# Optimization experiments

Hardware: AMD Instinct MI355X
Metric: run time of the kernel (lower is better)

Reference implementation:

```python
import jax, jax.numpy as jnp
import numpy as np
from jax import lax


def _lstm_layer(x_tmajor, Wi, Wh, b, c0, h0):
    """Run one LSTM layer over time-major input [T, B, F_in].

    Flax OptimizedLSTMCell math, gate order (i, f, g, o):
      gates = x @ Wi + h @ Wh + b
      c' = sigmoid(f) * c + sigmoid(i) * tanh(g)
      h' = sigmoid(o) * tanh(c')
    """
    F = Wh.shape[0]

    def step(carry, xt):
        c, h = carry
        gates = xt @ Wi + h @ Wh + b  # [B, 4F]
        i, f, g, o = jnp.split(gates, 4, axis=-1)
        c_new = jax.nn.sigmoid(f) * c + jax.nn.sigmoid(i) * jnp.tanh(g)
        h_new = jax.nn.sigmoid(o) * jnp.tanh(c_new)
        return (c_new, h_new), h_new

    (c_fin, h_fin), ys = lax.scan(step, (c0, h0), x_tmajor)
    return ys, c_fin, h_fin


def setup_inputs() -> dict:
    key = jax.random.key(0)
    kx, kwi, kwh = jax.random.split(key, 3)
    B, T, F, L = 16, 512, 1024, 2
    scale = 1.0 / np.sqrt(F)
    x = jax.random.normal(kx, (B, T, F), dtype=jnp.float32)
    Wi = jax.random.normal(kwi, (L, F, 4 * F), dtype=jnp.float32) * scale
    Wh = jax.random.normal(kwh, (L, F, 4 * F), dtype=jnp.float32) * scale
    b = jnp.zeros((L, 4 * F), dtype=jnp.float32)
    c0 = jnp.zeros((L, B, F), dtype=jnp.float32)
    h0 = jnp.zeros((L, B, F), dtype=jnp.float32)
    return {"x": x, "Wi": Wi, "Wh": Wh, "b": b, "c0": c0, "h0": h0}


def reference(x, Wi, Wh, b, c0, h0):
    # x: [B, T, F] -> time-major [T, B, F] for scan
    L = Wi.shape[0]
    h_seq = jnp.transpose(x, (1, 0, 2))
    c_finals, h_finals = [], []
    for l in range(L):  # small fixed layer count
        h_seq, c_f, h_f = _lstm_layer(h_seq, Wi[l], Wh[l], b[l], c0[l], h0[l])
        c_finals.append(c_f)
        h_finals.append(h_f)
    out = jnp.transpose(h_seq, (1, 0, 2))  # [B, T, F]
    return out, jnp.stack(c_finals), jnp.stack(h_finals)
```

## Files before the change

kernel.cpp:

```cpp
#include <hip/hip_runtime.h>

#define F1 1024
#define F4 4096
#define NB 16
#define NT 512
#define NWG 256

typedef float f32x4 __attribute__((ext_vector_type(4)));
typedef unsigned u32x4 __attribute__((ext_vector_type(4)));

__global__ __launch_bounds__(256) void gemm_xi(
    const float* __restrict__ A, const float* __restrict__ Wi,
    const float* __restrict__ bias, float* __restrict__ Xi, int a_batch_major)
{
    __shared__ __align__(16) float As[16][68];
    __shared__ __align__(16) float Bs[16][68];
    const int tid = threadIdx.x;
    const int n0 = blockIdx.x * 64;
    const int m0 = blockIdx.y * 64;

    const int lrow = tid >> 2, lkq = tid & 3;
    const int bkr = tid >> 4, bnq = tid & 15;
    const int tm = tid & 15, tn = tid >> 4;

    const int m_l = m0 + lrow;
    const float* arow;
    if (a_batch_major) {
        int t = m_l >> 4, b = m_l & 15;
        arow = A + (size_t)(b * NT + t) * F1;
    } else {
        arow = A + (size_t)m_l * F1;
    }

    float acc[4][4];
#pragma unroll
    for (int i = 0; i < 4; i++)
#pragma unroll
        for (int j = 0; j < 4; j++) acc[i][j] = 0.f;

    for (int kc = 0; kc < F1; kc += 16) {
        float4 a4 = *(const float4*)(arow + kc + lkq * 4);
        float4 b4 = *(const float4*)(Wi + (size_t)(kc + bkr) * F4 + n0 + bnq * 4);
        __syncthreads();
        As[lkq * 4 + 0][lrow] = a4.x;
        As[lkq * 4 + 1][lrow] = a4.y;
        As[lkq * 4 + 2][lrow] = a4.z;
        As[lkq * 4 + 3][lrow] = a4.w;
        *(float4*)&Bs[bkr][bnq * 4] = b4;
        __syncthreads();
#pragma unroll
        for (int k = 0; k < 16; k++) {
            const float4 av = *(const float4*)&As[k][tm * 4];
            const float4 bv = *(const float4*)&Bs[k][tn * 4];
            float a_[4] = {av.x, av.y, av.z, av.w};
            float b_[4] = {bv.x, bv.y, bv.z, bv.w};
#pragma unroll
            for (int i = 0; i < 4; i++)
#pragma unroll
                for (int j = 0; j < 4; j++)
                    acc[i][j] = fmaf(a_[i], b_[j], acc[i][j]);
        }
    }

    const int n = n0 + tn * 4;
    const int g = n >> 10;
    const int wgi = (n & 1023) >> 2;
    const int np = wgi * 16 + g * 4;
    const float4 bi = *(const float4*)(bias + n);
#pragma unroll
    for (int i = 0; i < 4; i++) {
        int m = m0 + tm * 4 + i;
        float4 o;
        o.x = acc[i][0] + bi.x;
        o.y = acc[i][1] + bi.y;
        o.z = acc[i][2] + bi.z;
        o.w = acc[i][3] + bi.w;
        *(float4*)(Xi + (size_t)m * F4 + np) = o;
    }
}

__global__ __launch_bounds__(512, 1) void lstm_recur(
    const float* __restrict__ Wh,
    const float* __restrict__ Xi,
    const float* __restrict__ c0,
    const float* __restrict__ h0,
    float* __restrict__ Hb,
    unsigned* __restrict__ flags,
    unsigned tbase,
    float* __restrict__ hseq,
    long long st_t, long long st_b,
    float* __restrict__ cfin, float* __restrict__ hfin)
{
    const int tid = threadIdx.x;
    const int wg = blockIdx.x;

    const int ks = tid >> 4;
    const int rb = (tid >> 2) & 3;
    const int g = tid & 3;

    __shared__ __align__(16) f32x4 hbuf4[16 * 257];
    __shared__ __align__(16) f32x4 red4[32 * 65];
    __shared__ float gbuf[16 * 20];

    float wh[32][4];
    {
        const float* wp = Wh + (size_t)(ks * 32) * F4 + g * F1 + wg * 4;
#pragma unroll
        for (int kk = 0; kk < 32; kk++) {
            float4 w4 = *(const float4*)(wp + (size_t)kk * F4);
            wh[kk][0] = w4.x; wh[kk][1] = w4.y; wh[kk][2] = w4.z; wh[kk][3] = w4.w;
        }
    }

    const int ab = tid >> 2, aj = tid & 3;
    float creg = 0.f;
    if (tid < 64) creg = c0[ab * F1 + wg * 4 + aj];

    for (int t = 0; t < NT; ++t) {
        f32x4 vv[8];
        if (t == 0) {
#pragma unroll
            for (int c = 0; c < 8; ++c) {
                int f4 = c * 512 + tid;
                vv[c] = *((const f32x4*)h0 + f4);
            }
        } else {
            const f32x4* hsrc = (const f32x4*)(Hb + (size_t)(t & 1) * (NB * F1));
#pragma unroll
            for (int c = 0; c < 8; ++c) {
                int f4 = c * 512 + tid;
                asm volatile("global_load_dwordx4 %0, %1, off sc1"
                             : "=v"(vv[c]) : "v"(hsrc + f4));
            }
            asm volatile("s_waitcnt vmcnt(0)" ::: "memory");
        }
#pragma unroll
        for (int c = 0; c < 8; ++c) {
            int f4 = c * 512 + tid;
            int r = f4 >> 8, k4 = f4 & 255;
            hbuf4[r * 257 + (k4 ^ ((k4 >> 3) & 7))] = vv[c];
        }
        float xiv = 0.f;
        if (tid < 256) {
            int r = tid >> 4, c = tid & 15;
            xiv = Xi[(size_t)(t * NB + r) * F4 + wg * 16 + c];
        }
        __syncthreads();

        float acc[4][4];
#pragma unroll
        for (int i = 0; i < 4; i++) {
            acc[i][0] = 0.f; acc[i][1] = 0.f; acc[i][2] = 0.f; acc[i][3] = 0.f;
        }
#pragma unroll
        for (int s = 0; s < 8; ++s) {
            const int k4 = (ks << 3) + s;
            const int slot = k4 ^ ((k4 >> 3) & 7);
            f32x4 hv[4];
#pragma unroll
            for (int i = 0; i < 4; i++) hv[i] = hbuf4[(rb * 4 + i) * 257 + slot];
#pragma unroll
            for (int i = 0; i < 4; i++) {
#pragma unroll
                for (int j = 0; j < 4; j++) {
                    acc[i][j] = fmaf(hv[i].x, wh[s * 4 + 0][j], acc[i][j]);
                    acc[i][j] = fmaf(hv[i].y, wh[s * 4 + 1][j], acc[i][j]);
                    acc[i][j] = fmaf(hv[i].z, wh[s * 4 + 2][j], acc[i][j]);
                    acc[i][j] = fmaf(hv[i].w, wh[s * 4 + 3][j], acc[i][j]);
                }
            }
        }
#pragma unroll
        for (int i = 0; i < 4; i++)
            red4[ks * 65 + (rb * 4 + i) * 4 + g] =
                (f32x4){acc[i][0], acc[i][1], acc[i][2], acc[i][3]};
        __syncthreads();

        if (tid < 256) {
            const float* rf = (const float*)red4;
            float s = xiv;
#pragma unroll
            for (int kss = 0; kss < 32; ++kss) s += rf[kss * 260 + tid];
            int r = tid >> 4, c = tid & 15;
            gbuf[r * 20 + c] = s;
        }
        __syncthreads();

        if (tid < 64) {
            float gi = gbuf[ab * 20 + 0 + aj];
            float gf = gbuf[ab * 20 + 4 + aj];
            float gg = gbuf[ab * 20 + 8 + aj];
            float go = gbuf[ab * 20 + 12 + aj];
            float si = 1.f / (1.f + __expf(-gi));
            float sf = 1.f / (1.f + __expf(-gf));
            float so = 1.f / (1.f + __expf(-go));
            float tg = 1.f - 2.f / (__expf(2.f * gg) + 1.f);
            float cn = sf * creg + si * tg;
            float tc = 1.f - 2.f / (__expf(2.f * cn) + 1.f);
            float hn = so * tc;
            creg = cn;
            int col = wg * 4 + aj;
            float* hp = Hb + (size_t)((t + 1) & 1) * (NB * F1) + ab * F1 + col;
            __hip_atomic_store(hp, hn, __ATOMIC_RELAXED, __HIP_MEMORY_SCOPE_AGENT);
            hseq[(size_t)t * st_t + (size_t)ab * st_b + col] = hn;
            if (t == NT - 1) {
                cfin[ab * F1 + col] = cn;
                hfin[ab * F1 + col] = hn;
            }
            asm volatile("s_waitcnt vmcnt(0)" ::: "memory");
        }
        if (tid == 0) {
            __hip_atomic_store(flags + wg, tbase + (unsigned)(t + 1),
                               __ATOMIC_RELAXED, __HIP_MEMORY_SCOPE_AGENT);
        }
        if (tid >= 448) {
            const unsigned target = tbase + (unsigned)(t + 1);
            const u32x4* fp = (const u32x4*)flags + (tid - 448);
            while (true) {
                u32x4 fv;
                asm volatile("global_load_dwordx4 %0, %1, off sc1"
                             : "=v"(fv) : "v"(fp));
                asm volatile("s_waitcnt vmcnt(0)" ::: "memory");
                int ok = (fv.x >= target) & (fv.y >= target) &
                         (fv.z >= target) & (fv.w >= target);
                if (__all(ok)) break;
            }
        }
        __syncthreads();
    }
}

extern "C" void kernel_launch(void* const* d_in, const int* in_sizes, int n_in,
                              void* d_out, int out_size, void* d_ws, size_t ws_size,
                              hipStream_t stream) {
    const float* x = (const float*)d_in[0];
    const float* Wi = (const float*)d_in[1];
    const float* Wh = (const float*)d_in[2];
    const float* bias = (const float*)d_in[3];
    const float* c0 = (const float*)d_in[4];
    const float* h0 = (const float*)d_in[5];
    float* out = (float*)d_out;

    float* Xi = (float*)d_ws;
    float* Hb = Xi + (size_t)8192 * 4096;
    unsigned* flags = (unsigned*)(Hb + 2 * NB * F1);

    float* hseq0 = out;
    float* cfin = out + (size_t)NB * NT * F1;
    float* hfin = cfin + 2 * NB * F1;

    const size_t lw = (size_t)F1 * F4;
    dim3 ggrid(64, 128), gblk(256);

    hipMemsetAsync(flags, 0, NWG * sizeof(unsigned), stream);

    gemm_xi<<<ggrid, gblk, 0, stream>>>(x, Wi, bias, Xi, 1);
    {
        const float* a0 = Wh;
        const float* a1 = Xi;
        const float* a2 = c0;
        const float* a3 = h0;
        float* a4 = Hb;
        unsigned* a5 = flags;
        unsigned a6 = 0;
        float* a7 = hseq0;
        long long a8 = (long long)NB * F1;
        long long a9 = F1;
        float* a10 = cfin;
        float* a11 = hfin;
        void* args[] = {&a0, &a1, &a2, &a3, &a4, &a5, &a6, &a7, &a8, &a9, &a10, &a11};
        hipLaunchCooperativeKernel((void*)lstm_recur, dim3(NWG), dim3(512), args, 0, stream);
    }
    gemm_xi<<<ggrid, gblk, 0, stream>>>(hseq0, Wi + lw, bias + F4, Xi, 0);
    {
        const float* a0 = Wh + lw;
        const float* a1 = Xi;
        const float* a2 = c0 + NB * F1;
        const float* a3 = h0 + NB * F1;
        float* a4 = Hb;
        unsigned* a5 = flags;
        unsigned a6 = (unsigned)NT;
        float* a7 = out;
        long long a8 = F1;
        long long a9 = (long long)NT * F1;
        float* a10 = cfin + NB * F1;
        float* a11 = hfin + NB * F1;
        void* args[] = {&a0, &a1, &a2, &a3, &a4, &a5, &a6, &a7, &a8, &a9, &a10, &a11};
        hipLaunchCooperativeKernel((void*)lstm_recur, dim3(NWG), dim3(512), args, 0, stream);
    }
}
```

Measured before the change: 10.72 ms.

## Use a centralized two-level grid barrier and read h directly from hseq

Replaces the all-to-all flag polling, where every workgroup scans all 256 flags, with a gather-and-release barrier. Workgroup 0 polls the arrival flags and then writes per-workgroup release words padded to separate cache lines. The other workgroups each spin on their own release word with a sleep, which cuts global polling traffic but adds a second hop to every step's barrier. The separate Hb double buffer is also dropped: h is stored once into hseq and the next step reads it from there. Those reads now use plain loads instead of sc1 loads, which risks reading stale cached data across workgroups.

```diff
diff --git a/kernel.cpp b/kernel.cpp
--- a/kernel.cpp
+++ b/kernel.cpp
@@ -84,8 +84,8 @@
     const float* __restrict__ Xi,
     const float* __restrict__ c0,
     const float* __restrict__ h0,
-    float* __restrict__ Hb,
     unsigned* __restrict__ flags,
+    unsigned* __restrict__ release,
     unsigned tbase,
     float* __restrict__ hseq,
     long long st_t, long long st_b,
@@ -117,22 +117,16 @@
     if (tid < 64) creg = c0[ab * F1 + wg * 4 + aj];
 
     for (int t = 0; t < NT; ++t) {
+        const float* hs;
+        long long rs;
+        if (t == 0) { hs = h0; rs = F1; }
+        else        { hs = hseq + (size_t)(t - 1) * st_t; rs = st_b; }
         f32x4 vv[8];
-        if (t == 0) {
-#pragma unroll
-            for (int c = 0; c < 8; ++c) {
-                int f4 = c * 512 + tid;
-                vv[c] = *((const f32x4*)h0 + f4);
-            }
-        } else {
-            const f32x4* hsrc = (const f32x4*)(Hb + (size_t)(t & 1) * (NB * F1));
-#pragma unroll
-            for (int c = 0; c < 8; ++c) {
-                int f4 = c * 512 + tid;
-                asm volatile("global_load_dwordx4 %0, %1, off sc1"
-                             : "=v"(vv[c]) : "v"(hsrc + f4));
-            }
-            asm volatile("s_waitcnt vmcnt(0)" ::: "memory");
+#pragma unroll
+        for (int c = 0; c < 8; ++c) {
+            int f4 = c * 512 + tid;
+            int r = f4 >> 8, k4 = f4 & 255;
+            vv[c] = *(const f32x4*)(hs + (size_t)r * rs + (size_t)k4 * 4);
         }
 #pragma unroll
         for (int c = 0; c < 8; ++c) {
@@ -200,9 +194,8 @@
             float hn = so * tc;
             creg = cn;
             int col = wg * 4 + aj;
-            float* hp = Hb + (size_t)((t + 1) & 1) * (NB * F1) + ab * F1 + col;
+            float* hp = hseq + (size_t)t * st_t + (size_t)ab * st_b + col;
             __hip_atomic_store(hp, hn, __ATOMIC_RELAXED, __HIP_MEMORY_SCOPE_AGENT);
-            hseq[(size_t)t * st_t + (size_t)ab * st_b + col] = hn;
             if (t == NT - 1) {
                 cfin[ab * F1 + col] = cn;
                 hfin[ab * F1 + col] = hn;
@@ -213,17 +206,38 @@
             __hip_atomic_store(flags + wg, tbase + (unsigned)(t + 1),
                                __ATOMIC_RELAXED, __HIP_MEMORY_SCOPE_AGENT);
         }
-        if (tid >= 448) {
-            const unsigned target = tbase + (unsigned)(t + 1);
-            const u32x4* fp = (const u32x4*)flags + (tid - 448);
-            while (true) {
-                u32x4 fv;
-                asm volatile("global_load_dwordx4 %0, %1, off sc1"
-                             : "=v"(fv) : "v"(fp));
-                asm volatile("s_waitcnt vmcnt(0)" ::: "memory");
-                int ok = (fv.x >= target) & (fv.y >= target) &
-                         (fv.z >= target) & (fv.w >= target);
-                if (__all(ok)) break;
+        const unsigned target = tbase + (unsigned)(t + 1);
+        if (wg == 0) {
+            if (tid >= 448) {
+                const int lane = tid - 448;
+                const u32x4* fp = (const u32x4*)flags + lane;
+                while (true) {
+                    u32x4 fv;
+                    asm volatile("global_load_dwordx4 %0, %1, off sc1"
+                                 : "=v"(fv) : "v"(fp));
+                    asm volatile("s_waitcnt vmcnt(0)" ::: "memory");
+                    int ok = (fv.x >= target) & (fv.y >= target) &
+                             (fv.z >= target) & (fv.w >= target);
+                    if (__all(ok)) break;
+                }
+#pragma unroll
+                for (int it = 0; it < 4; ++it) {
+                    unsigned* rp = release + (size_t)(it * 64 + lane) * 32;
+                    __hip_atomic_store(rp, target, __ATOMIC_RELAXED,
+                                       __HIP_MEMORY_SCOPE_AGENT);
+                }
+            }
+        } else {
+            if (tid == 448) {
+                const unsigned* rp = release + (size_t)wg * 32;
+                while (true) {
+                    unsigned v;
+                    asm volatile("global_load_dword %0, %1, off sc1"
+                                 : "=v"(v) : "v"(rp));
+                    asm volatile("s_waitcnt vmcnt(0)" ::: "memory");
+                    if (v >= target) break;
+                    asm volatile("s_sleep 1");
+                }
             }
         }
         __syncthreads();
@@ -242,8 +256,8 @@
     float* out = (float*)d_out;
 
     float* Xi = (float*)d_ws;
-    float* Hb = Xi + (size_t)8192 * 4096;
-    unsigned* flags = (unsigned*)(Hb + 2 * NB * F1);
+    unsigned* flags = (unsigned*)(Xi + (size_t)8192 * 4096);
+    unsigned* release = flags + NWG;
 
     float* hseq0 = out;
     float* cfin = out + (size_t)NB * NT * F1;
@@ -252,7 +266,7 @@
     const size_t lw = (size_t)F1 * F4;
     dim3 ggrid(64, 128), gblk(256);
 
-    hipMemsetAsync(flags, 0, NWG * sizeof(unsigned), stream);
+    hipMemsetAsync(flags, 0, (NWG + NWG * 32) * sizeof(unsigned), stream);
 
     gemm_xi<<<ggrid, gblk, 0, stream>>>(x, Wi, bias, Xi, 1);
     {
@@ -260,8 +274,8 @@
         const float* a1 = Xi;
         const float* a2 = c0;
         const float* a3 = h0;
-        float* a4 = Hb;
-        unsigned* a5 = flags;
+        unsigned* a4 = flags;
+        unsigned* a5 = release;
         unsigned a6 = 0;
         float* a7 = hseq0;
         long long a8 = (long long)NB * F1;
@@ -277,8 +291,8 @@
         const float* a1 = Xi;
         const float* a2 = c0 + NB * F1;
         const float* a3 = h0 + NB * F1;
-        float* a4 = Hb;
-        unsigned* a5 = flags;
+        unsigned* a4 = flags;
+        unsigned* a5 = release;
         unsigned a6 = (unsigned)NT;
         float* a7 = out;
         long long a8 = F1;
```

After: 9.172 ms. 14.4% less time.

## Fuse both LSTM layers into one wavefront-pipelined cooperative kernel

Applied to the files above, without the earlier changes.

Replaces the two sequential recurrent kernels and the layer-1 input GEMM with a single cooperative kernel. Each round computes the layer-0 step t and the layer-1 step t-1, computing the layer-1 input projection in-kernel from register-resident Wi1 weights. This removes one serial 512-step recurrence pass and one GEMM launch, at the cost of three times the per-step FMA work and register pressure per workgroup. Grid sync now uses per-round flags replicated 8 ways, so polling spreads across copies and the double-buffered h exchange goes away.

```diff
diff --git a/kernel.cpp b/kernel.cpp
--- a/kernel.cpp
+++ b/kernel.cpp
@@ -5,6 +5,8 @@
 #define NB 16
 #define NT 512
 #define NWG 256
+#define NR (NT + 1)
+#define EPM (NR * NWG)
 
 typedef float f32x4 __attribute__((ext_vector_type(4)));
 typedef unsigned u32x4 __attribute__((ext_vector_type(4)));
@@ -79,114 +81,182 @@
     }
 }
 
-__global__ __launch_bounds__(512, 1) void lstm_recur(
-    const float* __restrict__ Wh,
-    const float* __restrict__ Xi,
-    const float* __restrict__ c0,
-    const float* __restrict__ h0,
-    float* __restrict__ Hb,
-    unsigned* __restrict__ flags,
-    unsigned tbase,
-    float* __restrict__ hseq,
-    long long st_t, long long st_b,
+__global__ __launch_bounds__(512, 2) void lstm_fused(
+    const float* __restrict__ Wh0, const float* __restrict__ Wi1,
+    const float* __restrict__ Wh1, const float* __restrict__ b1,
+    const float* __restrict__ Xi0,
+    const float* __restrict__ c0in,
+    const float* __restrict__ h0in,
+    unsigned* __restrict__ ep,
+    float* __restrict__ h0seq,
+    float* __restrict__ out,
     float* __restrict__ cfin, float* __restrict__ hfin)
 {
     const int tid = threadIdx.x;
     const int wg = blockIdx.x;
-
-    const int ks = tid >> 4;
-    const int rb = (tid >> 2) & 3;
-    const int g = tid & 3;
+    const int ks = tid >> 2;
+    const int cg = tid & 3;
 
     __shared__ __align__(16) f32x4 hbuf4[16 * 257];
-    __shared__ __align__(16) f32x4 red4[32 * 65];
+    __shared__ __align__(16) f32x4 red4[256 * 17];
+    __shared__ __align__(16) f32x4 red2[512];
     __shared__ float gbuf[16 * 20];
 
-    float wh[32][4];
+    f32x4 wh0v[8], whxv[8], wh1v[8];
     {
-        const float* wp = Wh + (size_t)(ks * 32) * F4 + g * F1 + wg * 4;
-#pragma unroll
-        for (int kk = 0; kk < 32; kk++) {
-            float4 w4 = *(const float4*)(wp + (size_t)kk * F4);
-            wh[kk][0] = w4.x; wh[kk][1] = w4.y; wh[kk][2] = w4.z; wh[kk][3] = w4.w;
+        const size_t coff = (size_t)cg * F1 + wg * 4;
+        const float* p0 = Wh0 + (size_t)(ks * 8) * F4 + coff;
+        const float* px = Wi1 + (size_t)(ks * 8) * F4 + coff;
+        const float* p1 = Wh1 + (size_t)(ks * 8) * F4 + coff;
+#pragma unroll
+        for (int k = 0; k < 8; ++k) {
+            wh0v[k] = *(const f32x4*)(p0 + (size_t)k * F4);
+            whxv[k] = *(const f32x4*)(px + (size_t)k * F4);
+            wh1v[k] = *(const f32x4*)(p1 + (size_t)k * F4);
         }
     }
 
     const int ab = tid >> 2, aj = tid & 3;
-    float creg = 0.f;
-    if (tid < 64) creg = c0[ab * F1 + wg * 4 + aj];
-
-    for (int t = 0; t < NT; ++t) {
-        f32x4 vv[8];
-        if (t == 0) {
+    float c0reg = 0.f, c1reg = 0.f;
+    f32x4 b1v = {0.f, 0.f, 0.f, 0.f};
+    if (tid < 64) {
+        c0reg = c0in[ab * F1 + wg * 4 + aj];
+        c1reg = c0in[NB * F1 + ab * F1 + wg * 4 + aj];
+        b1v = *(const f32x4*)(b1 + (size_t)(tid & 3) * F1 + wg * 4);
+    }
+
+    for (int r = 0; r < NR; ++r) {
+        if (r > 0 && tid >= 448) {
+            const unsigned target = (unsigned)r;
+            const u32x4* fp = (const u32x4*)(ep + (size_t)(wg & 7) * EPM
+                                               + (size_t)(r - 1) * NWG) + (tid - 448);
+            while (true) {
+                u32x4 fv;
+                asm volatile("global_load_dwordx4 %0, %1, off sc1"
+                             : "=v"(fv) : "v"(fp));
+                asm volatile("s_waitcnt vmcnt(0)" ::: "memory");
+                int ok = (fv.x >= target) & (fv.y >= target) &
+                         (fv.z >= target) & (fv.w >= target);
+                if (__all(ok)) break;
+            }
+        }
+        __syncthreads();
+
+        f32x4 vv2[8];
+        f32x4 xi0v = {0.f, 0.f, 0.f, 0.f};
+        {
+            const float* hs0 = (r == 0) ? h0in
+                                        : (h0seq + (size_t)(r - 1) * (NB * F1));
+            f32x4 vv[8];
+#pragma unroll
+            for (int c = 0; c < 8; ++c)
+                vv[c] = *((const f32x4*)hs0 + c * 512 + tid);
+            if (r >= 1) {
+                if (r == 1) {
+                    const f32x4* hs1 = (const f32x4*)(h0in + NB * F1);
+#pragma unroll
+                    for (int c = 0; c < 8; ++c) vv2[c] = hs1[c * 512 + tid];
+                } else {
+                    const float* hs1 = out + (size_t)(r - 2) * F1;
+#pragma unroll
+                    for (int c = 0; c < 8; ++c) {
+                        int f4 = c * 512 + tid;
+                        vv2[c] = *(const f32x4*)(hs1
+                                   + (size_t)(f4 >> 8) * ((size_t)NT * F1)
+                                   + (size_t)(f4 & 255) * 4);
+                    }
+                }
+            }
+            if (tid < 64) {
+                int tX = (r < NT) ? r : NT - 1;
+                xi0v = *(const f32x4*)(Xi0 + (size_t)(tX * NB + ab) * F4
+                                           + wg * 16 + (tid & 3) * 4);
+            }
 #pragma unroll
             for (int c = 0; c < 8; ++c) {
                 int f4 = c * 512 + tid;
-                vv[c] = *((const f32x4*)h0 + f4);
-            }
-        } else {
-            const f32x4* hsrc = (const f32x4*)(Hb + (size_t)(t & 1) * (NB * F1));
+                int rr = f4 >> 8, k4 = f4 & 255;
+                hbuf4[rr * 257 + (k4 ^ ((k4 >> 3) & 7))] = vv[c];
+            }
+        }
+        __syncthreads();
+
+        f32x4 acc[16];
+#pragma unroll
+        for (int i = 0; i < 16; ++i) acc[i] = (f32x4){0.f, 0.f, 0.f, 0.f};
+#pragma unroll
+        for (int k4l = 0; k4l < 2; ++k4l) {
+            const int k4 = (ks << 1) + k4l;
+            const int slot = k4 ^ ((k4 >> 3) & 7);
+#pragma unroll
+            for (int rr = 0; rr < 16; ++rr) {
+                f32x4 hv = hbuf4[rr * 257 + slot];
+                acc[rr] += hv.x * wh0v[k4l * 4 + 0];
+                acc[rr] += hv.y * wh0v[k4l * 4 + 1];
+                acc[rr] += hv.z * wh0v[k4l * 4 + 2];
+                acc[rr] += hv.w * wh0v[k4l * 4 + 3];
+            }
+        }
+#pragma unroll
+        for (int rr = 0; rr < 16; ++rr) {
+            f32x4 o;
+            o.x = __shfl_xor(acc[rr].x, 4);
+            o.y = __shfl_xor(acc[rr].y, 4);
+            o.z = __shfl_xor(acc[rr].z, 4);
+            o.w = __shfl_xor(acc[rr].w, 4);
+            acc[rr] += o;
+        }
+        if ((ks & 1) == 0) {
+            const int base = ((ks >> 1) * 4 + cg) * 17;
+#pragma unroll
+            for (int rr = 0; rr < 16; ++rr) red4[base + rr] = acc[rr];
+        }
+        __syncthreads();
+
+        {
+            const int rw = tid >> 5, cgq = (tid >> 3) & 3, kq = tid & 7;
+            f32x4 s = {0.f, 0.f, 0.f, 0.f};
+#pragma unroll
+            for (int j = 0; j < 8; ++j)
+                s += red4[((kq * 8 + j) * 4 + cgq) * 17 + rw];
+            red2[(rw * 4 + cgq) * 8 + kq] = s;
+        }
+        __syncthreads();
+
+        if (tid < 64) {
+            f32x4 s = xi0v;
+#pragma unroll
+            for (int kq = 0; kq < 8; ++kq) s += red2[tid * 8 + kq];
+            *(f32x4*)&gbuf[(tid >> 2) * 20 + (tid & 3) * 4] = s;
+        }
+#pragma unroll
+        for (int i = 0; i < 16; ++i) acc[i] = (f32x4){0.f, 0.f, 0.f, 0.f};
+        if (r >= 1) {
+#pragma unroll
+            for (int k4l = 0; k4l < 2; ++k4l) {
+                const int k4 = (ks << 1) + k4l;
+                const int slot = k4 ^ ((k4 >> 3) & 7);
+#pragma unroll
+                for (int rr = 0; rr < 16; ++rr) {
+                    f32x4 hv = hbuf4[rr * 257 + slot];
+                    acc[rr] += hv.x * whxv[k4l * 4 + 0];
+                    acc[rr] += hv.y * whxv[k4l * 4 + 1];
+                    acc[rr] += hv.z * whxv[k4l * 4 + 2];
+                    acc[rr] += hv.w * whxv[k4l * 4 + 3];
+                }
+            }
+        }
+        __syncthreads();
+
+        if (r >= 1) {
 #pragma unroll
             for (int c = 0; c < 8; ++c) {
                 int f4 = c * 512 + tid;
-                asm volatile("global_load_dwordx4 %0, %1, off sc1"
-                             : "=v"(vv[c]) : "v"(hsrc + f4));
-            }
-            asm volatile("s_waitcnt vmcnt(0)" ::: "memory");
-        }
-#pragma unroll
-        for (int c = 0; c < 8; ++c) {
-            int f4 = c * 512 + tid;
-            int r = f4 >> 8, k4 = f4 & 255;
-            hbuf4[r * 257 + (k4 ^ ((k4 >> 3) & 7))] = vv[c];
-        }
-        float xiv = 0.f;
-        if (tid < 256) {
-            int r = tid >> 4, c = tid & 15;
-            xiv = Xi[(size_t)(t * NB + r) * F4 + wg * 16 + c];
-        }
-        __syncthreads();
-
-        float acc[4][4];
-#pragma unroll
-        for (int i = 0; i < 4; i++) {
-            acc[i][0] = 0.f; acc[i][1] = 0.f; acc[i][2] = 0.f; acc[i][3] = 0.f;
-        }
-#pragma unroll
-        for (int s = 0; s < 8; ++s) {
-            const int k4 = (ks << 3) + s;
-            const int slot = k4 ^ ((k4 >> 3) & 7);
-            f32x4 hv[4];
-#pragma unroll
-            for (int i = 0; i < 4; i++) hv[i] = hbuf4[(rb * 4 + i) * 257 + slot];
-#pragma unroll
-            for (int i = 0; i < 4; i++) {
-#pragma unroll
-                for (int j = 0; j < 4; j++) {
-                    acc[i][j] = fmaf(hv[i].x, wh[s * 4 + 0][j], acc[i][j]);
-                    acc[i][j] = fmaf(hv[i].y, wh[s * 4 + 1][j], acc[i][j]);
-                    acc[i][j] = fmaf(hv[i].z, wh[s * 4 + 2][j], acc[i][j]);
-                    acc[i][j] = fmaf(hv[i].w, wh[s * 4 + 3][j], acc[i][j]);
-                }
-            }
-        }
-#pragma unroll
-        for (int i = 0; i < 4; i++)
-            red4[ks * 65 + (rb * 4 + i) * 4 + g] =
-                (f32x4){acc[i][0], acc[i][1], acc[i][2], acc[i][3]};
-        __syncthreads();
-
-        if (tid < 256) {
-            const float* rf = (const float*)red4;
-            float s = xiv;
-#pragma unroll
-            for (int kss = 0; kss < 32; ++kss) s += rf[kss * 260 + tid];
-            int r = tid >> 4, c = tid & 15;
-            gbuf[r * 20 + c] = s;
-        }
-        __syncthreads();
-
-        if (tid < 64) {
+                int rr = f4 >> 8, k4 = f4 & 255;
+                hbuf4[rr * 257 + (k4 ^ ((k4 >> 3) & 7))] = vv2[c];
+            }
+        }
+        if (tid < 64 && r < NT) {
             float gi = gbuf[ab * 20 + 0 + aj];
             float gf = gbuf[ab * 20 + 4 + aj];
             float gg = gbuf[ab * 20 + 8 + aj];
@@ -195,38 +265,96 @@
             float sf = 1.f / (1.f + __expf(-gf));
             float so = 1.f / (1.f + __expf(-go));
             float tg = 1.f - 2.f / (__expf(2.f * gg) + 1.f);
-            float cn = sf * creg + si * tg;
+            float cn = sf * c0reg + si * tg;
             float tc = 1.f - 2.f / (__expf(2.f * cn) + 1.f);
             float hn = so * tc;
-            creg = cn;
-            int col = wg * 4 + aj;
-            float* hp = Hb + (size_t)((t + 1) & 1) * (NB * F1) + ab * F1 + col;
+            c0reg = cn;
+            float* hp = h0seq + (size_t)r * (NB * F1) + ab * F1 + wg * 4 + aj;
             __hip_atomic_store(hp, hn, __ATOMIC_RELAXED, __HIP_MEMORY_SCOPE_AGENT);
-            hseq[(size_t)t * st_t + (size_t)ab * st_b + col] = hn;
-            if (t == NT - 1) {
-                cfin[ab * F1 + col] = cn;
-                hfin[ab * F1 + col] = hn;
+            if (r == NT - 1) {
+                cfin[ab * F1 + wg * 4 + aj] = cn;
+                hfin[ab * F1 + wg * 4 + aj] = hn;
+            }
+        }
+        __syncthreads();
+
+        if (r >= 1) {
+#pragma unroll
+            for (int k4l = 0; k4l < 2; ++k4l) {
+                const int k4 = (ks << 1) + k4l;
+                const int slot = k4 ^ ((k4 >> 3) & 7);
+#pragma unroll
+                for (int rr = 0; rr < 16; ++rr) {
+                    f32x4 hv = hbuf4[rr * 257 + slot];
+                    acc[rr] += hv.x * wh1v[k4l * 4 + 0];
+                    acc[rr] += hv.y * wh1v[k4l * 4 + 1];
+                    acc[rr] += hv.z * wh1v[k4l * 4 + 2];
+                    acc[rr] += hv.w * wh1v[k4l * 4 + 3];
+                }
+            }
+#pragma unroll
+            for (int rr = 0; rr < 16; ++rr) {
+                f32x4 o;
+                o.x = __shfl_xor(acc[rr].x, 4);
+                o.y = __shfl_xor(acc[rr].y, 4);
+                o.z = __shfl_xor(acc[rr].z, 4);
+                o.w = __shfl_xor(acc[rr].w, 4);
+                acc[rr] += o;
+            }
+            if ((ks & 1) == 0) {
+                const int base = ((ks >> 1) * 4 + cg) * 17;
+#pragma unroll
+                for (int rr = 0; rr < 16; ++rr) red4[base + rr] = acc[rr];
+            }
+        }
+        __syncthreads();
+
+        if (r >= 1) {
+            const int rw = tid >> 5, cgq = (tid >> 3) & 3, kq = tid & 7;
+            f32x4 s = {0.f, 0.f, 0.f, 0.f};
+#pragma unroll
+            for (int j = 0; j < 8; ++j)
+                s += red4[((kq * 8 + j) * 4 + cgq) * 17 + rw];
+            red2[(rw * 4 + cgq) * 8 + kq] = s;
+        }
+        __syncthreads();
+
+        if (r >= 1 && tid < 64) {
+            f32x4 s = b1v;
+#pragma unroll
+            for (int kq = 0; kq < 8; ++kq) s += red2[tid * 8 + kq];
+            *(f32x4*)&gbuf[(tid >> 2) * 20 + (tid & 3) * 4] = s;
+        }
+        __syncthreads();
+
+        if (tid < 64) {
+            if (r >= 1) {
+                float gi = gbuf[ab * 20 + 0 + aj];
+                float gf = gbuf[ab * 20 + 4 + aj];
+                float gg = gbuf[ab * 20 + 8 + aj];
+                float go = gbuf[ab * 20 + 12 + aj];
+                float si = 1.f / (1.f + __expf(-gi));
+                float sf = 1.f / (1.f + __expf(-gf));
+                float so = 1.f / (1.f + __expf(-go));
+                float tg = 1.f - 2.f / (__expf(2.f * gg) + 1.f);
+                float cn = sf * c1reg + si * tg;
+                float tc = 1.f - 2.f / (__expf(2.f * cn) + 1.f);
+                float hn = so * tc;
+                c1reg = cn;
+                float* hp = out + (size_t)ab * ((size_t)NT * F1)
+                                + (size_t)(r - 1) * F1 + wg * 4 + aj;
+                __hip_atomic_store(hp, hn, __ATOMIC_RELAXED, __HIP_MEMORY_SCOPE_AGENT);
+                if (r == NT) {
+                    cfin[NB * F1 + ab * F1 + wg * 4 + aj] = cn;
+                    hfin[NB * F1 + ab * F1 + wg * 4 + aj] = hn;
+                }
             }
             asm volatile("s_waitcnt vmcnt(0)" ::: "memory");
-        }
-        if (tid == 0) {
-            __hip_atomic_store(flags + wg, tbase + (unsigned)(t + 1),
-                               __ATOMIC_RELAXED, __HIP_MEMORY_SCOPE_AGENT);
-        }
-        if (tid >= 448) {
-            const unsigned target = tbase + (unsigned)(t + 1);
-            const u32x4* fp = (const u32x4*)flags + (tid - 448);
-            while (true) {
-                u32x4 fv;
-                asm volatile("global_load_dwordx4 %0, %1, off sc1"
-                             : "=v"(fv) : "v"(fp));
-                asm volatile("s_waitcnt vmcnt(0)" ::: "memory");
-                int ok = (fv.x >= target) & (fv.y >= target) &
-                         (fv.z >= target) & (fv.w >= target);
-                if (__all(ok)) break;
-            }
-        }
-        __syncthreads();
+            if (tid < 8)
+                __hip_atomic_store(ep + (size_t)tid * EPM + (size_t)r * NWG + wg,
+                                   (unsigned)(r + 1), __ATOMIC_RELAXED,
+                                   __HIP_MEMORY_SCOPE_AGENT);
+        }
     }
 }
 
@@ -241,51 +369,33 @@
     const float* h0 = (const float*)d_in[5];
     float* out = (float*)d_out;
 
-    float* Xi = (float*)d_ws;
-    float* Hb = Xi + (size_t)8192 * 4096;
-    unsigned* flags = (unsigned*)(Hb + 2 * NB * F1);
-
-    float* hseq0 = out;
+    float* Xi0 = (float*)d_ws;
+    float* h0seq = Xi0 + (size_t)NT * NB * F4;
+    unsigned* ep = (unsigned*)(h0seq + (size_t)NT * NB * F1);
+
     float* cfin = out + (size_t)NB * NT * F1;
     float* hfin = cfin + 2 * NB * F1;
 
     const size_t lw = (size_t)F1 * F4;
-    dim3 ggrid(64, 128), gblk(256);
-
-    hipMemsetAsync(flags, 0, NWG * sizeof(unsigned), stream);
-
-    gemm_xi<<<ggrid, gblk, 0, stream>>>(x, Wi, bias, Xi, 1);
+
+    hipMemsetAsync(ep, 0, (size_t)8 * EPM * sizeof(unsigned), stream);
+
+    gemm_xi<<<dim3(64, 128), dim3(256), 0, stream>>>(x, Wi, bias, Xi0, 1);
+
     {
         const float* a0 = Wh;
-        const float* a1 = Xi;
-        const float* a2 = c0;
-        const float* a3 = h0;
-        float* a4 = Hb;
-        unsigned* a5 = flags;
-        unsigned a6 = 0;
-        float* a7 = hseq0;
-        long long a8 = (long long)NB * F1;
-        long long a9 = F1;
+        const float* a1 = Wi + lw;
+        const float* a2 = Wh + lw;
+        const float* a3 = bias + F4;
+        const float* a4 = Xi0;
+        const float* a5 = c0;
+        const float* a6 = h0;
+        unsigned* a7 = ep;
+        float* a8 = h0seq;
+        float* a9 = out;
         float* a10 = cfin;
         float* a11 = hfin;
         void* args[] = {&a0, &a1, &a2, &a3, &a4, &a5, &a6, &a7, &a8, &a9, &a10, &a11};
-        hipLaunchCooperativeKernel((void*)lstm_recur, dim3(NWG), dim3(512), args, 0, stream);
-    }
-    gemm_xi<<<ggrid, gblk, 0, stream>>>(hseq0, Wi + lw, bias + F4, Xi, 0);
-    {
-        const float* a0 = Wh + lw;
-        const float* a1 = Xi;
-        const float* a2 = c0 + NB * F1;
-        const float* a3 = h0 + NB * F1;
-        float* a4 = Hb;
-        unsigned* a5 = flags;
-        unsigned a6 = (unsigned)NT;
-        float* a7 = out;
-        long long a8 = F1;
-        long long a9 = (long long)NT * F1;
-        float* a10 = cfin + NB * F1;
-        float* a11 = hfin + NB * F1;
-        void* args[] = {&a0, &a1, &a2, &a3, &a4, &a5, &a6, &a7, &a8, &a9, &a10, &a11};
-        hipLaunchCooperativeKernel((void*)lstm_recur, dim3(NWG), dim3(512), args, 0, stream);
+        hipLaunchCooperativeKernel((void*)lstm_fused, dim3(NWG), dim3(512), args, 0, stream);
     }
 }
```

New measurement: 11.44 ms. 1.07x slower.
